# Optimization experiments

Measured on AMD Instinct MI355X. Metric: run time of the kernel, lower is better.

The kernel has to match this reference:

```python
import jax, jax.numpy as jnp
import numpy as np

D_MODEL = 1024
NUM_HEADS = 16
MAX_LEN = 2048
D_HEAD = D_MODEL // NUM_HEADS
BATCH = 2
SEQ = 2048


def setup_inputs() -> dict:
    key = jax.random.key(0)
    ks = jax.random.split(key, 8)
    s = 1.0 / np.sqrt(D_MODEL)
    return {
        "x": jax.random.normal(ks[0], (BATCH, SEQ, D_MODEL), dtype=jnp.float32),
        "Wq": jax.random.uniform(ks[1], (D_MODEL, D_MODEL), jnp.float32, -s, s),
        "bq": jax.random.uniform(ks[2], (D_MODEL,), jnp.float32, -s, s),
        "Wk": jax.random.uniform(ks[3], (D_MODEL, D_MODEL), jnp.float32, -s, s),
        "bk": jax.random.uniform(ks[4], (D_MODEL,), jnp.float32, -s, s),
        "Wv": jax.random.uniform(ks[5], (D_MODEL, D_MODEL), jnp.float32, -s, s),
        "bv": jax.random.uniform(ks[6], (D_MODEL,), jnp.float32, -s, s),
        "Er": jax.random.normal(ks[7], (MAX_LEN, D_HEAD), dtype=jnp.float32),
    }


def _skew(QEr):
    # QEr: [B, H, S, S]  (music-transformer skew trick)
    B, H, S, _ = QEr.shape
    padded = jnp.pad(QEr, ((0, 0), (0, 0), (0, 0), (1, 0)))  # [B,H,S,S+1]
    reshaped = padded.reshape(B, H, S + 1, S)
    return reshaped[:, :, 1:, :]  # [B,H,S,S]


def reference(x, Wq, bq, Wk, bk, Wv, bv, Er):
    B, S, D = x.shape
    H, Dh = NUM_HEADS, D_HEAD
    # projections (torch Linear: x @ W.T + b)
    q = (jnp.einsum('bsd,ed->bse', x, Wq) + bq).reshape(B, S, H, Dh).transpose(0, 2, 1, 3)
    k = (jnp.einsum('bsd,ed->bse', x, Wk) + bk).reshape(B, S, H, Dh).transpose(0, 2, 1, 3)
    v = (jnp.einsum('bsd,ed->bse', x, Wv) + bv).reshape(B, S, H, Dh).transpose(0, 2, 1, 3)
    # relative position scores
    Er_slice = Er[MAX_LEN - S:, :]                    # [S, Dh]
    QEr = jnp.einsum('bhsd,td->bhst', q, Er_slice)    # [B,H,S,S]
    Srel = _skew(QEr)
    QKt = jnp.einsum('bhsd,bhtd->bhst', q, k)
    attn = (QKt + Srel) / jnp.sqrt(jnp.asarray(Dh, x.dtype))
    causal = jnp.tril(jnp.ones((S, S), dtype=bool))
    attn = jnp.where(causal[None, None], attn, -jnp.inf)
    attn = jax.nn.softmax(attn, axis=-1)
    out = jnp.einsum('bhst,bhtd->bhsd', attn, v)      # [B,H,S,Dh]
    out = out.transpose(0, 2, 1, 3).reshape(B, S, D)
    return out  # dropout is identity in eval mode
```

## Files before the change

kernel.cpp:

```cpp
#include <hip/hip_runtime.h>
#include <hip/hip_bf16.h>

constexpr int B  = 2;
constexpr int S  = 2048;
constexpr int D  = 1024;
constexpr int H  = 16;

typedef unsigned short u16t;
typedef unsigned long long u64;
typedef __attribute__((ext_vector_type(8))) short short8;
typedef __attribute__((ext_vector_type(4))) float float4v;

__device__ __forceinline__ float b2f(unsigned int u) {
    union { unsigned int i; float f; } c; c.i = u << 16; return c.f;
}
__device__ __forceinline__ u16t f2b(float f) {
    __hip_bfloat16 h = __float2bfloat16(f);
    union { __hip_bfloat16 h; u16t u; } c; c.h = h; return c.u;
}
__device__ __forceinline__ unsigned int pkbf(float a, float b) {
    return (unsigned int)f2b(a) | ((unsigned int)f2b(b) << 16);
}
__device__ __forceinline__ u64 pack4(float4 v) {
    return (u64)f2b(v.x) | ((u64)f2b(v.y) << 16) | ((u64)f2b(v.z) << 32) | ((u64)f2b(v.w) << 48);
}

typedef __attribute__((address_space(1))) const unsigned int* as1_u32p;
typedef __attribute__((address_space(3))) unsigned int* as3_u32p;
__device__ __forceinline__ void gll16(const void* g, void* l) {
    __builtin_amdgcn_global_load_lds((as1_u32p)g, (as3_u32p)l, 16, 0, 0);
}

constexpr size_t XB_OFF = 0;
constexpr size_t WQ_OFF = 4194304;
constexpr size_t WK_OFF = 5242880;
constexpr size_t WV_OFF = 6291456;
constexpr size_t ER_OFF = 7340032;
constexpr size_t QW_OFF = 7471104;
constexpr size_t KW_OFF = 11665408;
constexpr size_t VT_OFF = 15859712;

__global__ __launch_bounds__(256) void prep_bf16(
    const float* __restrict__ x,  const float* __restrict__ Wq,
    const float* __restrict__ Wk, const float* __restrict__ Wv,
    const float* __restrict__ Er, u64* __restrict__ dst)
{
    size_t i4 = (size_t)blockIdx.x * 256 + threadIdx.x;
    const float* src; size_t off;
    if      (i4 < 1048576) { src = x;  off = i4; }
    else if (i4 < 1310720) { src = Wq; off = i4 - 1048576; }
    else if (i4 < 1572864) { src = Wk; off = i4 - 1310720; }
    else if (i4 < 1835008) { src = Wv; off = i4 - 1572864; }
    else                   { src = Er; off = i4 - 1835008; }
    float4 v = ((const float4*)src)[off];
    dst[i4] = pack4(v);
}

__global__ __launch_bounds__(256, 3) void qkv_mfma(
    const u16t* __restrict__ xb,
    const u16t* __restrict__ wqb, const u16t* __restrict__ wkb, const u16t* __restrict__ wvb,
    const float* __restrict__ bq, const float* __restrict__ bk, const float* __restrict__ bv,
    u16t* __restrict__ qo, u16t* __restrict__ ko, u16t* __restrict__ vT)
{
    const int z = blockIdx.z;
    const u16t*  W    = (z == 0) ? wqb : (z == 1) ? wkb : wvb;
    const float* bias = (z == 0) ? bq  : (z == 1) ? bk  : bv;

    __shared__ __align__(16) u16t Xs[128][72];
    __shared__ __align__(16) u16t Ws[128][72];

    const int tid = threadIdx.x;
    const int w = tid >> 6, lane = tid & 63;
    const int quad = lane >> 4, l16 = lane & 15;
    const int m0 = blockIdx.x * 128, n0 = blockIdx.y * 128;
    const int mi = (w >> 1) * 64, ni = (w & 1) * 64;

    float4v acc[4][4];
    #pragma unroll
    for (int mt = 0; mt < 4; ++mt)
        #pragma unroll
        for (int nt = 0; nt < 4; ++nt) acc[mt][nt] = (float4v){0.f, 0.f, 0.f, 0.f};

    short8 xa[4], wa[4];
    #pragma unroll
    for (int it = 0; it < 4; ++it) {
        int idx = tid + it * 256, r = idx >> 3, c = idx & 7;
        xa[it] = *(const short8*)&xb[(size_t)(m0 + r) * D + c * 8];
        wa[it] = *(const short8*)&W [(size_t)(n0 + r) * D + c * 8];
    }

    for (int k0 = 0; k0 < D; k0 += 64) {
        __syncthreads();
        #pragma unroll
        for (int it = 0; it < 4; ++it) {
            int idx = tid + it * 256, r = idx >> 3, c = idx & 7;
            *(short8*)&Xs[r][c * 8] = xa[it];
            *(short8*)&Ws[r][c * 8] = wa[it];
        }
        __syncthreads();
        if (k0 + 64 < D) {
            #pragma unroll
            for (int it = 0; it < 4; ++it) {
                int idx = tid + it * 256, r = idx >> 3, c = idx & 7;
                xa[it] = *(const short8*)&xb[(size_t)(m0 + r) * D + k0 + 64 + c * 8];
                wa[it] = *(const short8*)&W [(size_t)(n0 + r) * D + k0 + 64 + c * 8];
            }
        }
        short8 af[4][2], bf[4][2];
        #pragma unroll
        for (int mt = 0; mt < 4; ++mt) {
            af[mt][0] = *(const short8*)&Xs[mi + mt * 16 + l16][quad * 8];
            af[mt][1] = *(const short8*)&Xs[mi + mt * 16 + l16][quad * 8 + 32];
        }
        #pragma unroll
        for (int nt = 0; nt < 4; ++nt) {
            bf[nt][0] = *(const short8*)&Ws[ni + nt * 16 + l16][quad * 8];
            bf[nt][1] = *(const short8*)&Ws[ni + nt * 16 + l16][quad * 8 + 32];
        }
        #pragma unroll
        for (int mt = 0; mt < 4; ++mt)
            #pragma unroll
            for (int nt = 0; nt < 4; ++nt) {
                acc[mt][nt] = __builtin_amdgcn_mfma_f32_16x16x32_bf16(af[mt][0], bf[nt][0], acc[mt][nt], 0, 0, 0);
                acc[mt][nt] = __builtin_amdgcn_mfma_f32_16x16x32_bf16(af[mt][1], bf[nt][1], acc[mt][nt], 0, 0, 0);
            }
    }

    float bias_v[4];
    #pragma unroll
    for (int nt = 0; nt < 4; ++nt) bias_v[nt] = bias[n0 + ni + nt * 16 + l16];

    #pragma unroll
    for (int mt = 0; mt < 4; ++mt)
        #pragma unroll
        for (int nt = 0; nt < 4; ++nt) {
            int n = n0 + ni + nt * 16 + l16;
            int h = n >> 6, dh = n & 63;
            int mb = m0 + mi + mt * 16 + quad * 4;
            int b_ = mb >> 11, s = mb & (S - 1);
            if (z == 2) {
                float4 o;
                o.x = acc[mt][nt][0] + bias_v[nt];
                o.y = acc[mt][nt][1] + bias_v[nt];
                o.z = acc[mt][nt][2] + bias_v[nt];
                o.w = acc[mt][nt][3] + bias_v[nt];
                *(u64*)&vT[((size_t)(b_ * H + h) * 64 + dh) * S + s] = pack4(o);
            } else {
                u16t* out = (z == 0) ? qo : ko;
                #pragma unroll
                for (int rg = 0; rg < 4; ++rg)
                    out[((size_t)(b_ * H + h) * S + s + rg) * 64 + dh] =
                        f2b(acc[mt][nt][rg] + bias_v[nt]);
            }
        }
}

__global__ __launch_bounds__(256, 4) void attn_mfma(
    const u16t* __restrict__ q, const u16t* __restrict__ k,
    const u16t* __restrict__ vT, const u16t* __restrict__ er,
    float* __restrict__ out)
{
    __shared__ __align__(16) u16t KsS[2][64 * 64];
    __shared__ __align__(16) u16t VsS[2][64 * 64];
    __shared__ __align__(16) u16t PsS[64 * 64];
    __shared__ float lrows[64];
    char* KsB = (char*)KsS;
    char* VsB = (char*)VsS;
    char* PsB = (char*)PsS;

    const int tid = threadIdx.x;
    const int w = tid >> 6, lane = tid & 63;
    const int quad = lane >> 4, l16 = lane & 15;
    const int bh = blockIdx.x;
    const int pr = blockIdx.y;
    const int hh = bh & (H - 1), bb = bh >> 4;

    const u16t* qb = q  + (size_t)bh * S * 64;
    const u16t* kb = k  + (size_t)bh * S * 64;
    const u16t* vb = vT + (size_t)bh * 64 * S;

    const int xk = (l16 & 7);
    const float SC = 0.18033688f;
    const float M2 = 17.3125f;

    const int srow = lane >> 3;
    const int d8s  = (lane & 7) ^ (srow & 7);

    #pragma unroll 1
    for (int ph = 0; ph < 2; ++ph) {
        const int ix = ph ? (31 - pr) : pr;
        const int s0 = ix * 64;

        const size_t qoff = (size_t)(s0 + w * 16 + l16) * 64;
        const short8 Qa0 = *(const short8*)&qb[qoff + quad * 8];
        const short8 Qa1 = *(const short8*)&qb[qoff + 32 + quad * 8];

        float4v accO[4], L[5];
        #pragma unroll
        for (int t = 0; t < 4; ++t) accO[t] = (float4v){0.f, 0.f, 0.f, 0.f};
        float lsum[4] = {0.f, 0.f, 0.f, 0.f};

        #pragma unroll
        for (int it = 0; it < 2; ++it) {
            int ci = w * 2 + it;
            int prow = ci * 8 + srow;
            gll16(&kb[(size_t)prow * 64 + d8s * 8], KsB + ci * 1024);
            gll16(&vb[(size_t)prow * S + d8s * 8], VsB + ci * 1024);
        }
        __syncthreads();

        for (int jt = 0; jt <= ix; ++jt) {
            const int t0 = jt * 64;
            const int jbase = S - 64 - s0 + t0;
            const bool diag = (jt == ix);
            const int bsel = (jt & 1) * 8192;

            short8 ef0[4], ef1[4], e00, e01;
            #pragma unroll
            for (int c = 1; c <= 4; ++c) {
                int grow = jbase + (3 - w + c) * 16 + l16;
                if (grow > S - 1) grow = S - 1;
                const u16t* ep = &er[(size_t)grow * 64 + quad * 8];
                ef0[c - 1] = *(const short8*)ep;
                ef1[c - 1] = *(const short8*)(ep + 32);
            }
            if (jt == 0) {
                int grow = jbase + (3 - w) * 16 + l16;
                if (grow > S - 1) grow = S - 1;
                const u16t* ep = &er[(size_t)grow * 64 + quad * 8];
                e00 = *(const short8*)ep;
                e01 = *(const short8*)(ep + 32);
            }

            if (jt < ix) {
                int nb = ((jt + 1) & 1) * 8192;
                #pragma unroll
                for (int it = 0; it < 2; ++it) {
                    int ci = w * 2 + it;
                    int prow = ci * 8 + srow;
                    gll16(&kb[(size_t)(t0 + 64 + prow) * 64 + d8s * 8], KsB + nb + ci * 1024);
                    gll16(&vb[(size_t)prow * S + t0 + 64 + d8s * 8], VsB + nb + ci * 1024);
                }
            }

            float4v S1[4];
            #pragma unroll
            for (int nt = 0; nt < 4; ++nt) {
                int row = nt * 16 + l16;
                short8 b0 = *(const short8*)(KsB + bsel + row * 128 + ((quad ^ xk) << 4));
                short8 b1 = *(const short8*)(KsB + bsel + row * 128 + (((quad + 4) ^ xk) << 4));
                float4v a = (float4v){0.f, 0.f, 0.f, 0.f};
                a = __builtin_amdgcn_mfma_f32_16x16x32_bf16(Qa0, b0, a, 0, 0, 0);
                a = __builtin_amdgcn_mfma_f32_16x16x32_bf16(Qa1, b1, a, 0, 0, 0);
                S1[nt] = a;
            }

            if (jt == 0) {
                float4v e = (float4v){0.f, 0.f, 0.f, 0.f};
                e = __builtin_amdgcn_mfma_f32_16x16x32_bf16(Qa0, e00, e, 0, 0, 0);
                e = __builtin_amdgcn_mfma_f32_16x16x32_bf16(Qa1, e01, e, 0, 0, 0);
                L[0] = e;
            } else {
                L[0] = L[4];
            }
            #pragma unroll
            for (int c = 1; c <= 4; ++c) {
                float4v e = (float4v){0.f, 0.f, 0.f, 0.f};
                e = __builtin_amdgcn_mfma_f32_16x16x32_bf16(Qa0, ef0[c - 1], e, 0, 0, 0);
                e = __builtin_amdgcn_mfma_f32_16x16x32_bf16(Qa1, ef1[c - 1], e, 0, 0, 0);
                L[c] = e;
            }

            #pragma unroll
            for (int rg = 0; rg < 4; ++rg) {
                const int usel = quad * 4 + rg;
                const int thr = 15 - usel;
                const int sidx = ((lane & 48) | ((l16 + thr) & 15)) * 4;
                const bool give_lo = (l16 >= thr);
                unsigned int p01 = give_lo ? pkbf(L[0][rg], L[1][rg]) : pkbf(L[1][rg], L[2][rg]);
                unsigned int p23 = give_lo ? pkbf(L[2][rg], L[3][rg]) : pkbf(L[3][rg], L[4][rg]);
                unsigned int q01 = (unsigned int)__builtin_amdgcn_ds_bpermute(sidx, (int)p01);
                unsigned int q23 = (unsigned int)__builtin_amdgcn_ds_bpermute(sidx, (int)p23);
                float qe[4] = { b2f(q01 & 0xffffu), b2f(q01 >> 16),
                                b2f(q23 & 0xffffu), b2f(q23 >> 16) };
                const int i_ = w * 16 + usel;
                const int ikey = i_ & 7;
                float psum = 0.f;
                #pragma unroll
                for (int nt = 0; nt < 4; ++nt) {
                    float s2 = fmaf(S1[nt][rg] + qe[nt], SC, -M2);
                    float p = (diag && (nt * 16 + l16 > i_)) ? 0.f : exp2f(s2);
                    psum += p;
                    int j_ = nt * 16 + l16;
                    *(u16t*)(PsB + i_ * 128 + (((j_ >> 3) ^ ikey) << 4) + (j_ & 7) * 2) = f2b(p);
                }
                lsum[rg] += psum;
            }

            {
                int ar = w * 16 + l16;
                short8 pa0 = *(const short8*)(PsB + ar * 128 + ((quad ^ (ar & 7)) << 4));
                short8 pa1 = *(const short8*)(PsB + ar * 128 + (((quad + 4) ^ (ar & 7)) << 4));
                #pragma unroll
                for (int td = 0; td < 4; ++td) {
                    int row = td * 16 + l16;
                    short8 a0 = *(const short8*)(VsB + bsel + row * 128 + ((quad ^ xk) << 4));
                    short8 a1 = *(const short8*)(VsB + bsel + row * 128 + (((quad + 4) ^ xk) << 4));
                    accO[td] = __builtin_amdgcn_mfma_f32_16x16x32_bf16(a0, pa0, accO[td], 0, 0, 0);
                    accO[td] = __builtin_amdgcn_mfma_f32_16x16x32_bf16(a1, pa1, accO[td], 0, 0, 0);
                }
            }
            __syncthreads();
        }

        #pragma unroll
        for (int rg = 0; rg < 4; ++rg) {
            float s = lsum[rg];
            s += __shfl_xor(s, 1);
            s += __shfl_xor(s, 2);
            s += __shfl_xor(s, 4);
            s += __shfl_xor(s, 8);
            if (l16 == 0) lrows[w * 16 + quad * 4 + rg] = s;
        }
        float inv = 1.f / lrows[w * 16 + l16];

        float* ob = out + (size_t)bb * S * D + (size_t)hh * 64
                    + (size_t)(s0 + w * 16 + l16) * D;
        #pragma unroll
        for (int td = 0; td < 4; ++td) {
            float4 o;
            o.x = accO[td][0] * inv;
            o.y = accO[td][1] * inv;
            o.z = accO[td][2] * inv;
            o.w = accO[td][3] * inv;
            *(float4*)&ob[td * 16 + quad * 4] = o;
        }
    }
}

extern "C" void kernel_launch(void* const* d_in, const int* in_sizes, int n_in,
                              void* d_out, int out_size, void* d_ws, size_t ws_size,
                              hipStream_t stream) {
    const float* x  = (const float*)d_in[0];
    const float* Wq = (const float*)d_in[1];
    const float* bq = (const float*)d_in[2];
    const float* Wk = (const float*)d_in[3];
    const float* bk = (const float*)d_in[4];
    const float* Wv = (const float*)d_in[5];
    const float* bv = (const float*)d_in[6];
    const float* Er = (const float*)d_in[7];
    float* out = (float*)d_out;

    u16t* ws16 = (u16t*)d_ws;
    u16t* xb  = ws16 + XB_OFF;
    u16t* wqb = ws16 + WQ_OFF;
    u16t* wkb = ws16 + WK_OFF;
    u16t* wvb = ws16 + WV_OFF;
    u16t* erb = ws16 + ER_OFF;
    u16t* qw  = ws16 + QW_OFF;
    u16t* kw  = ws16 + KW_OFF;
    u16t* vTw = ws16 + VT_OFF;

    prep_bf16<<<dim3(7296), dim3(256), 0, stream>>>(x, Wq, Wk, Wv, Er, (u64*)d_ws);

    qkv_mfma<<<dim3(32, 8, 3), dim3(256), 0, stream>>>(
        xb, wqb, wkb, wvb, bq, bk, bv, qw, kw, vTw);

    attn_mfma<<<dim3(32, 16), dim3(256), 0, stream>>>(qw, kw, vTw, erb, out);
}
```

Baseline: 203.1 us.

## Split attention into one-tile blocks ordered heavy-first; use direct-to-LDS loads in QKV GEMM

The attention kernel used to give each block two paired query tiles (ix and 31-ix). Now each block handles one 64-row query tile, and 1024 blocks are launched in an order that puts the longest causal rows first. This is meant to improve occupancy and tail balance, though each K/V tile is now reused across fewer query rows. The QKV GEMM replaces register staging plus padded LDS with global_load_lds into XOR-swizzled LDS. That drops the register prefetch, so global latency is no longer overlapped with MFMA work. The lrows buffer now aliases the P buffer in shared memory.

```diff
diff --git a/kernel.cpp b/kernel.cpp
--- a/kernel.cpp
+++ b/kernel.cpp
@@ -66,8 +66,10 @@
     const u16t*  W    = (z == 0) ? wqb : (z == 1) ? wkb : wvb;
     const float* bias = (z == 0) ? bq  : (z == 1) ? bk  : bv;
 
-    __shared__ __align__(16) u16t Xs[128][72];
-    __shared__ __align__(16) u16t Ws[128][72];
+    __shared__ __align__(16) u16t Xs[128 * 64];
+    __shared__ __align__(16) u16t Ws[128 * 64];
+    char* XsB = (char*)Xs;
+    char* WsB = (char*)Ws;
 
     const int tid = threadIdx.x;
     const int w = tid >> 6, lane = tid & 63;
@@ -75,47 +77,38 @@
     const int m0 = blockIdx.x * 128, n0 = blockIdx.y * 128;
     const int mi = (w >> 1) * 64, ni = (w & 1) * 64;
 
+    const int srow = lane >> 3;
+    const int d8s  = (lane & 7) ^ (srow & 7);
+    const int xk   = l16 & 7;
+
     float4v acc[4][4];
     #pragma unroll
     for (int mt = 0; mt < 4; ++mt)
         #pragma unroll
         for (int nt = 0; nt < 4; ++nt) acc[mt][nt] = (float4v){0.f, 0.f, 0.f, 0.f};
 
-    short8 xa[4], wa[4];
-    #pragma unroll
-    for (int it = 0; it < 4; ++it) {
-        int idx = tid + it * 256, r = idx >> 3, c = idx & 7;
-        xa[it] = *(const short8*)&xb[(size_t)(m0 + r) * D + c * 8];
-        wa[it] = *(const short8*)&W [(size_t)(n0 + r) * D + c * 8];
-    }
-
     for (int k0 = 0; k0 < D; k0 += 64) {
+        #pragma unroll
+        for (int it = 0; it < 4; ++it) {
+            int ci  = w * 4 + it;
+            int row = ci * 8 + srow;
+            gll16(&xb[(size_t)(m0 + row) * D + k0 + d8s * 8], XsB + ci * 1024);
+            gll16(&W [(size_t)(n0 + row) * D + k0 + d8s * 8], WsB + ci * 1024);
+        }
         __syncthreads();
-        #pragma unroll
-        for (int it = 0; it < 4; ++it) {
-            int idx = tid + it * 256, r = idx >> 3, c = idx & 7;
-            *(short8*)&Xs[r][c * 8] = xa[it];
-            *(short8*)&Ws[r][c * 8] = wa[it];
-        }
-        __syncthreads();
-        if (k0 + 64 < D) {
-            #pragma unroll
-            for (int it = 0; it < 4; ++it) {
-                int idx = tid + it * 256, r = idx >> 3, c = idx & 7;
-                xa[it] = *(const short8*)&xb[(size_t)(m0 + r) * D + k0 + 64 + c * 8];
-                wa[it] = *(const short8*)&W [(size_t)(n0 + r) * D + k0 + 64 + c * 8];
-            }
-        }
+
         short8 af[4][2], bf[4][2];
         #pragma unroll
         for (int mt = 0; mt < 4; ++mt) {
-            af[mt][0] = *(const short8*)&Xs[mi + mt * 16 + l16][quad * 8];
-            af[mt][1] = *(const short8*)&Xs[mi + mt * 16 + l16][quad * 8 + 32];
+            int r = mi + mt * 16 + l16;
+            af[mt][0] = *(const short8*)(XsB + r * 128 + ((quad       ^ xk) << 4));
+            af[mt][1] = *(const short8*)(XsB + r * 128 + (((quad + 4) ^ xk) << 4));
         }
         #pragma unroll
         for (int nt = 0; nt < 4; ++nt) {
-            bf[nt][0] = *(const short8*)&Ws[ni + nt * 16 + l16][quad * 8];
-            bf[nt][1] = *(const short8*)&Ws[ni + nt * 16 + l16][quad * 8 + 32];
+            int r = ni + nt * 16 + l16;
+            bf[nt][0] = *(const short8*)(WsB + r * 128 + ((quad       ^ xk) << 4));
+            bf[nt][1] = *(const short8*)(WsB + r * 128 + (((quad + 4) ^ xk) << 4));
         }
         #pragma unroll
         for (int mt = 0; mt < 4; ++mt)
@@ -124,6 +117,7 @@
                 acc[mt][nt] = __builtin_amdgcn_mfma_f32_16x16x32_bf16(af[mt][0], bf[nt][0], acc[mt][nt], 0, 0, 0);
                 acc[mt][nt] = __builtin_amdgcn_mfma_f32_16x16x32_bf16(af[mt][1], bf[nt][1], acc[mt][nt], 0, 0, 0);
             }
+        __syncthreads();
     }
 
     float bias_v[4];
@@ -163,16 +157,23 @@
     __shared__ __align__(16) u16t KsS[2][64 * 64];
     __shared__ __align__(16) u16t VsS[2][64 * 64];
     __shared__ __align__(16) u16t PsS[64 * 64];
-    __shared__ float lrows[64];
     char* KsB = (char*)KsS;
     char* VsB = (char*)VsS;
     char* PsB = (char*)PsS;
+    float* lrows = (float*)PsS;
 
     const int tid = threadIdx.x;
     const int w = tid >> 6, lane = tid & 63;
     const int quad = lane >> 4, l16 = lane & 15;
-    const int bh = blockIdx.x;
-    const int pr = blockIdx.y;
+
+    const int r_  = blockIdx.x;
+    const int g   = blockIdx.y;
+    const int bh  = r_ & 31;
+    const int slot = r_ >> 5;
+    const int ix  = (g == 0) ? (31 - slot)
+                  : (g == 1) ? (16 + slot)
+                  : (g == 2) ? (15 - slot)
+                  :            slot;
     const int hh = bh & (H - 1), bb = bh >> 4;
 
     const u16t* qb = q  + (size_t)bh * S * 64;
@@ -186,155 +187,151 @@
     const int srow = lane >> 3;
     const int d8s  = (lane & 7) ^ (srow & 7);
 
-    #pragma unroll 1
-    for (int ph = 0; ph < 2; ++ph) {
-        const int ix = ph ? (31 - pr) : pr;
-        const int s0 = ix * 64;
-
-        const size_t qoff = (size_t)(s0 + w * 16 + l16) * 64;
-        const short8 Qa0 = *(const short8*)&qb[qoff + quad * 8];
-        const short8 Qa1 = *(const short8*)&qb[qoff + 32 + quad * 8];
-
-        float4v accO[4], L[5];
-        #pragma unroll
-        for (int t = 0; t < 4; ++t) accO[t] = (float4v){0.f, 0.f, 0.f, 0.f};
-        float lsum[4] = {0.f, 0.f, 0.f, 0.f};
-
-        #pragma unroll
-        for (int it = 0; it < 2; ++it) {
-            int ci = w * 2 + it;
-            int prow = ci * 8 + srow;
-            gll16(&kb[(size_t)prow * 64 + d8s * 8], KsB + ci * 1024);
-            gll16(&vb[(size_t)prow * S + d8s * 8], VsB + ci * 1024);
-        }
-        __syncthreads();
-
-        for (int jt = 0; jt <= ix; ++jt) {
-            const int t0 = jt * 64;
-            const int jbase = S - 64 - s0 + t0;
-            const bool diag = (jt == ix);
-            const int bsel = (jt & 1) * 8192;
-
-            short8 ef0[4], ef1[4], e00, e01;
+    const int s0 = ix * 64;
+
+    const size_t qoff = (size_t)(s0 + w * 16 + l16) * 64;
+    const short8 Qa0 = *(const short8*)&qb[qoff + quad * 8];
+    const short8 Qa1 = *(const short8*)&qb[qoff + 32 + quad * 8];
+
+    float4v accO[4], L[5];
+    #pragma unroll
+    for (int t = 0; t < 4; ++t) accO[t] = (float4v){0.f, 0.f, 0.f, 0.f};
+    float lsum[4] = {0.f, 0.f, 0.f, 0.f};
+
+    #pragma unroll
+    for (int it = 0; it < 2; ++it) {
+        int ci = w * 2 + it;
+        int prow = ci * 8 + srow;
+        gll16(&kb[(size_t)prow * 64 + d8s * 8], KsB + ci * 1024);
+        gll16(&vb[(size_t)prow * S + d8s * 8], VsB + ci * 1024);
+    }
+    __syncthreads();
+
+    for (int jt = 0; jt <= ix; ++jt) {
+        const int t0 = jt * 64;
+        const int jbase = S - 64 - s0 + t0;
+        const bool diag = (jt == ix);
+        const int bsel = (jt & 1) * 8192;
+
+        short8 ef0[4], ef1[4], e00, e01;
+        #pragma unroll
+        for (int c = 1; c <= 4; ++c) {
+            int grow = jbase + (3 - w + c) * 16 + l16;
+            if (grow > S - 1) grow = S - 1;
+            const u16t* ep = &er[(size_t)grow * 64 + quad * 8];
+            ef0[c - 1] = *(const short8*)ep;
+            ef1[c - 1] = *(const short8*)(ep + 32);
+        }
+        if (jt == 0) {
+            int grow = jbase + (3 - w) * 16 + l16;
+            if (grow > S - 1) grow = S - 1;
+            const u16t* ep = &er[(size_t)grow * 64 + quad * 8];
+            e00 = *(const short8*)ep;
+            e01 = *(const short8*)(ep + 32);
+        }
+
+        if (jt < ix) {
+            int nb = ((jt + 1) & 1) * 8192;
             #pragma unroll
-            for (int c = 1; c <= 4; ++c) {
-                int grow = jbase + (3 - w + c) * 16 + l16;
-                if (grow > S - 1) grow = S - 1;
-                const u16t* ep = &er[(size_t)grow * 64 + quad * 8];
-                ef0[c - 1] = *(const short8*)ep;
-                ef1[c - 1] = *(const short8*)(ep + 32);
-            }
-            if (jt == 0) {
-                int grow = jbase + (3 - w) * 16 + l16;
-                if (grow > S - 1) grow = S - 1;
-                const u16t* ep = &er[(size_t)grow * 64 + quad * 8];
-                e00 = *(const short8*)ep;
-                e01 = *(const short8*)(ep + 32);
-            }
-
-            if (jt < ix) {
-                int nb = ((jt + 1) & 1) * 8192;
-                #pragma unroll
-                for (int it = 0; it < 2; ++it) {
-                    int ci = w * 2 + it;
-                    int prow = ci * 8 + srow;
-                    gll16(&kb[(size_t)(t0 + 64 + prow) * 64 + d8s * 8], KsB + nb + ci * 1024);
-                    gll16(&vb[(size_t)prow * S + t0 + 64 + d8s * 8], VsB + nb + ci * 1024);
-                }
-            }
-
-            float4v S1[4];
+            for (int it = 0; it < 2; ++it) {
+                int ci = w * 2 + it;
+                int prow = ci * 8 + srow;
+                gll16(&kb[(size_t)(t0 + 64 + prow) * 64 + d8s * 8], KsB + nb + ci * 1024);
+                gll16(&vb[(size_t)prow * S + t0 + 64 + d8s * 8], VsB + nb + ci * 1024);
+            }
+        }
+
+        float4v S1[4];
+        #pragma unroll
+        for (int nt = 0; nt < 4; ++nt) {
+            int row = nt * 16 + l16;
+            short8 b0 = *(const short8*)(KsB + bsel + row * 128 + ((quad ^ xk) << 4));
+            short8 b1 = *(const short8*)(KsB + bsel + row * 128 + (((quad + 4) ^ xk) << 4));
+            float4v a = (float4v){0.f, 0.f, 0.f, 0.f};
+            a = __builtin_amdgcn_mfma_f32_16x16x32_bf16(Qa0, b0, a, 0, 0, 0);
+            a = __builtin_amdgcn_mfma_f32_16x16x32_bf16(Qa1, b1, a, 0, 0, 0);
+            S1[nt] = a;
+        }
+
+        if (jt == 0) {
+            float4v e = (float4v){0.f, 0.f, 0.f, 0.f};
+            e = __builtin_amdgcn_mfma_f32_16x16x32_bf16(Qa0, e00, e, 0, 0, 0);
+            e = __builtin_amdgcn_mfma_f32_16x16x32_bf16(Qa1, e01, e, 0, 0, 0);
+            L[0] = e;
+        } else {
+            L[0] = L[4];
+        }
+        #pragma unroll
+        for (int c = 1; c <= 4; ++c) {
+            float4v e = (float4v){0.f, 0.f, 0.f, 0.f};
+            e = __builtin_amdgcn_mfma_f32_16x16x32_bf16(Qa0, ef0[c - 1], e, 0, 0, 0);
+            e = __builtin_amdgcn_mfma_f32_16x16x32_bf16(Qa1, ef1[c - 1], e, 0, 0, 0);
+            L[c] = e;
+        }
+
+        #pragma unroll
+        for (int rg = 0; rg < 4; ++rg) {
+            const int usel = quad * 4 + rg;
+            const int thr = 15 - usel;
+            const int sidx = ((lane & 48) | ((l16 + thr) & 15)) * 4;
+            const bool give_lo = (l16 >= thr);
+            unsigned int p01 = give_lo ? pkbf(L[0][rg], L[1][rg]) : pkbf(L[1][rg], L[2][rg]);
+            unsigned int p23 = give_lo ? pkbf(L[2][rg], L[3][rg]) : pkbf(L[3][rg], L[4][rg]);
+            unsigned int q01 = (unsigned int)__builtin_amdgcn_ds_bpermute(sidx, (int)p01);
+            unsigned int q23 = (unsigned int)__builtin_amdgcn_ds_bpermute(sidx, (int)p23);
+            float qe[4] = { b2f(q01 & 0xffffu), b2f(q01 >> 16),
+                            b2f(q23 & 0xffffu), b2f(q23 >> 16) };
+            const int i_ = w * 16 + usel;
+            const int ikey = i_ & 7;
+            float psum = 0.f;
             #pragma unroll
             for (int nt = 0; nt < 4; ++nt) {
-                int row = nt * 16 + l16;
-                short8 b0 = *(const short8*)(KsB + bsel + row * 128 + ((quad ^ xk) << 4));
-                short8 b1 = *(const short8*)(KsB + bsel + row * 128 + (((quad + 4) ^ xk) << 4));
-                float4v a = (float4v){0.f, 0.f, 0.f, 0.f};
-                a = __builtin_amdgcn_mfma_f32_16x16x32_bf16(Qa0, b0, a, 0, 0, 0);
-                a = __builtin_amdgcn_mfma_f32_16x16x32_bf16(Qa1, b1, a, 0, 0, 0);
-                S1[nt] = a;
-            }
-
-            if (jt == 0) {
-                float4v e = (float4v){0.f, 0.f, 0.f, 0.f};
-                e = __builtin_amdgcn_mfma_f32_16x16x32_bf16(Qa0, e00, e, 0, 0, 0);
-                e = __builtin_amdgcn_mfma_f32_16x16x32_bf16(Qa1, e01, e, 0, 0, 0);
-                L[0] = e;
-            } else {
-                L[0] = L[4];
-            }
+                float s2 = fmaf(S1[nt][rg] + qe[nt], SC, -M2);
+                float p = (diag && (nt * 16 + l16 > i_)) ? 0.f : exp2f(s2);
+                psum += p;
+                int j_ = nt * 16 + l16;
+                *(u16t*)(PsB + i_ * 128 + (((j_ >> 3) ^ ikey) << 4) + (j_ & 7) * 2) = f2b(p);
+            }
+            lsum[rg] += psum;
+        }
+
+        {
+            int ar = w * 16 + l16;
+            short8 pa0 = *(const short8*)(PsB + ar * 128 + ((quad ^ (ar & 7)) << 4));
+            short8 pa1 = *(const short8*)(PsB + ar * 128 + (((quad + 4) ^ (ar & 7)) << 4));
             #pragma unroll
-            for (int c = 1; c <= 4; ++c) {
-                float4v e = (float4v){0.f, 0.f, 0.f, 0.f};
-                e = __builtin_amdgcn_mfma_f32_16x16x32_bf16(Qa0, ef0[c - 1], e, 0, 0, 0);
-                e = __builtin_amdgcn_mfma_f32_16x16x32_bf16(Qa1, ef1[c - 1], e, 0, 0, 0);
-                L[c] = e;
-            }
-
-            #pragma unroll
-            for (int rg = 0; rg < 4; ++rg) {
-                const int usel = quad * 4 + rg;
-                const int thr = 15 - usel;
-                const int sidx = ((lane & 48) | ((l16 + thr) & 15)) * 4;
-                const bool give_lo = (l16 >= thr);
-                unsigned int p01 = give_lo ? pkbf(L[0][rg], L[1][rg]) : pkbf(L[1][rg], L[2][rg]);
-                unsigned int p23 = give_lo ? pkbf(L[2][rg], L[3][rg]) : pkbf(L[3][rg], L[4][rg]);
-                unsigned int q01 = (unsigned int)__builtin_amdgcn_ds_bpermute(sidx, (int)p01);
-                unsigned int q23 = (unsigned int)__builtin_amdgcn_ds_bpermute(sidx, (int)p23);
-                float qe[4] = { b2f(q01 & 0xffffu), b2f(q01 >> 16),
-                                b2f(q23 & 0xffffu), b2f(q23 >> 16) };
-                const int i_ = w * 16 + usel;
-                const int ikey = i_ & 7;
-                float psum = 0.f;
-                #pragma unroll
-                for (int nt = 0; nt < 4; ++nt) {
-                    float s2 = fmaf(S1[nt][rg] + qe[nt], SC, -M2);
-                    float p = (diag && (nt * 16 + l16 > i_)) ? 0.f : exp2f(s2);
-                    psum += p;
-                    int j_ = nt * 16 + l16;
-                    *(u16t*)(PsB + i_ * 128 + (((j_ >> 3) ^ ikey) << 4) + (j_ & 7) * 2) = f2b(p);
-                }
-                lsum[rg] += psum;
-            }
-
-            {
-                int ar = w * 16 + l16;
-                short8 pa0 = *(const short8*)(PsB + ar * 128 + ((quad ^ (ar & 7)) << 4));
-                short8 pa1 = *(const short8*)(PsB + ar * 128 + (((quad + 4) ^ (ar & 7)) << 4));
-                #pragma unroll
-                for (int td = 0; td < 4; ++td) {
-                    int row = td * 16 + l16;
-                    short8 a0 = *(const short8*)(VsB + bsel + row * 128 + ((quad ^ xk) << 4));
-                    short8 a1 = *(const short8*)(VsB + bsel + row * 128 + (((quad + 4) ^ xk) << 4));
-                    accO[td] = __builtin_amdgcn_mfma_f32_16x16x32_bf16(a0, pa0, accO[td], 0, 0, 0);
-                    accO[td] = __builtin_amdgcn_mfma_f32_16x16x32_bf16(a1, pa1, accO[td], 0, 0, 0);
-                }
-            }
-            __syncthreads();
-        }
-
-        #pragma unroll
-        for (int rg = 0; rg < 4; ++rg) {
-            float s = lsum[rg];
-            s += __shfl_xor(s, 1);
-            s += __shfl_xor(s, 2);
-            s += __shfl_xor(s, 4);
-            s += __shfl_xor(s, 8);
-            if (l16 == 0) lrows[w * 16 + quad * 4 + rg] = s;
-        }
-        float inv = 1.f / lrows[w * 16 + l16];
-
-        float* ob = out + (size_t)bb * S * D + (size_t)hh * 64
-                    + (size_t)(s0 + w * 16 + l16) * D;
-        #pragma unroll
-        for (int td = 0; td < 4; ++td) {
-            float4 o;
-            o.x = accO[td][0] * inv;
-            o.y = accO[td][1] * inv;
-            o.z = accO[td][2] * inv;
-            o.w = accO[td][3] * inv;
-            *(float4*)&ob[td * 16 + quad * 4] = o;
-        }
+            for (int td = 0; td < 4; ++td) {
+                int row = td * 16 + l16;
+                short8 a0 = *(const short8*)(VsB + bsel + row * 128 + ((quad ^ xk) << 4));
+                short8 a1 = *(const short8*)(VsB + bsel + row * 128 + (((quad + 4) ^ xk) << 4));
+                accO[td] = __builtin_amdgcn_mfma_f32_16x16x32_bf16(a0, pa0, accO[td], 0, 0, 0);
+                accO[td] = __builtin_amdgcn_mfma_f32_16x16x32_bf16(a1, pa1, accO[td], 0, 0, 0);
+            }
+        }
+        __syncthreads();
+    }
+
+    #pragma unroll
+    for (int rg = 0; rg < 4; ++rg) {
+        float s = lsum[rg];
+        s += __shfl_xor(s, 1);
+        s += __shfl_xor(s, 2);
+        s += __shfl_xor(s, 4);
+        s += __shfl_xor(s, 8);
+        if (l16 == 0) lrows[w * 16 + quad * 4 + rg] = s;
+    }
+    float inv = 1.f / lrows[w * 16 + l16];
+
+    float* ob = out + (size_t)bb * S * D + (size_t)hh * 64
+                + (size_t)(s0 + w * 16 + l16) * D;
+    #pragma unroll
+    for (int td = 0; td < 4; ++td) {
+        float4 o;
+        o.x = accO[td][0] * inv;
+        o.y = accO[td][1] * inv;
+        o.z = accO[td][2] * inv;
+        o.w = accO[td][3] * inv;
+        *(float4*)&ob[td * 16 + quad * 4] = o;
     }
 }
 
@@ -366,5 +363,5 @@
     qkv_mfma<<<dim3(32, 8, 3), dim3(256), 0, stream>>>(
         xb, wqb, wkb, wvb, bq, bk, bv, qw, kw, vTw);
 
-    attn_mfma<<<dim3(32, 16), dim3(256), 0, stream>>>(qw, kw, vTw, erb, out);
-}
+    attn_mfma<<<dim3(256, 4), dim3(256), 0, stream>>>(qw, kw, vTw, erb, out);
+}
```

New measurement: 200.5 us. About the same (-1.3%).
